# Kernel optimization log

Measured on AMD Instinct MI355X. Metric: run time of the kernel, lower is better.

The kernel has to match this reference:

```python
import jax, jax.numpy as jnp
import numpy as np

MAX_TIMESTEPS = 6
K_WTA = 1
THR_RATE = 0.05
OUT_CHANNELS = 128
TARGET_RATE = K_WTA / OUT_CHANNELS


def setup_inputs() -> dict:
    key = jax.random.key(0)
    kx, kw = jax.random.split(key)
    x = jax.random.normal(kx, (8, 128, 64, 64), dtype=jnp.float32)
    W = jax.random.normal(kw, (128, 256, 11, 11), dtype=jnp.float32)
    # per-output-filter L2 normalization as in __init__
    W = W / (1e-10 + jnp.sqrt(jnp.sum(W * W, axis=(1, 2, 3), keepdims=True)))
    return {"x": x, "W": W}


def _conv_same(x_in, W):
    return jax.lax.conv_general_dilated(
        x_in, W, window_strides=(1, 1), padding="SAME",
        dimension_numbers=("NCHW", "OIHW", "NCHW"))


def reference(x, W):
    B, C, H, Wd = x.shape
    Cout = W.shape[0]

    z0 = jnp.zeros((B, Cout, H, Wd), dtype=x.dtype)  # zeros_like(x), channels match
    b0 = jnp.zeros((1, Cout, 1, 1), dtype=x.dtype)

    def step(carry, t):
        z_prev, b = carry
        x_in = jnp.concatenate([x, z_prev], axis=1)          # [B, 2C, H, W]
        prelimy = _conv_same(x_in, W)                         # [B, Cout, H, W]
        realy = prelimy - b
        # EMA blend with previous (binarized) activation for t > 0
        realy = jnp.where(t > 0, 0.5 * realy + 0.5 * z_prev, realy)
        # k-WTA with k=1 over channel dim: keep only per-pixel channel max, binarize
        thr = jnp.max(realy, axis=1, keepdims=True)
        masked = jnp.where(realy < thr, 0.0, realy)
        z = (masked > 0).astype(x.dtype)
        # running sparsity-controlled bias update
        rate = jnp.mean(z, axis=(0, 2, 3)).reshape(1, -1, 1, 1)
        b = b + THR_RATE * (rate - TARGET_RATE)
        x_in_new = jnp.concatenate([x, z], axis=1)
        change = jnp.mean(jnp.abs(x_in - x_in_new))           # F.l1_loss
        return (z, b), (change, z)

    (_, _), (changes, zs) = jax.lax.scan(step, (z0, b0), jnp.arange(MAX_TIMESTEPS))
    features = jnp.transpose(zs, (1, 0, 2, 3, 4))             # [B, T, Cout, H, W]
    return changes, features
```

## Files before the change

### kernel.cpp

```cpp
#include <hip/hip_runtime.h>

typedef double d4 __attribute__((ext_vector_type(4)));

static constexpr int BN = 8;
static constexpr int CX = 128;
static constexpr int CO = 128;
static constexpr int HH = 64;
static constexpr int WW = 64;
static constexpr int KT = 121;
static constexpr int NPIX = HH * WW;
static constexpr int TOTPIX = BN * NPIX;

__global__ __launch_bounds__(128) void k_wt(const float* __restrict__ W,
                                            float* __restrict__ WxT,
                                            float* __restrict__ WzT) {
  int blk  = blockIdx.x;
  int part = blk >> 7;
  int ci   = blk & 127;
  int co   = threadIdx.x;
  const float* src = &W[((co * 256) + part * 128 + ci) * KT];
  float* dst = (part ? WzT : WxT) + ci * KT * 128 + co;
#pragma unroll 11
  for (int k = 0; k < KT; ++k) dst[k * 128] = src[k];
}

__global__ __launch_bounds__(256, 4) void k_conv(const float* __restrict__ x,
                                                 const float* __restrict__ WxT,
                                                 double* __restrict__ base) {
  int blk = blockIdx.x;
  int cog = blk & 7;
  int wt  = (blk >> 3) & 3;
  int ht  = (blk >> 5) & 3;
  int b   = blk >> 7;
  int H0 = ht * 16, W0 = wt * 16, CO0 = cog * 16;

  int tid  = threadIdx.x;
  int lane = tid & 63;
  int wv   = tid >> 6;
  int lg   = lane >> 4;
  int lc   = lane & 15;

  __shared__ double xs[42 * 28];
  __shared__ double wsl[124 * 16];
  __shared__ unsigned offtbl[124];

  if (tid < 124) {
    unsigned off;
    if (tid < 121) {
      int ki = tid / 11, kj = tid - ki * 11;
      off = (unsigned)(ki * 28 + kj);
    } else {
      off = (unsigned)(26 * 28);
    }
    offtbl[tid] = off;
  }
  for (int e = tid; e < 42 * 28; e += 256) xs[e] = 0.0;
  if (tid < 48) wsl[121 * 16 + tid] = 0.0;

  d4 zz = {0., 0., 0., 0.};
  double amu  = (double)lc;
  double bsel = (lg == 0) ? 1.0 : 0.0;
  d4 pr = __builtin_amdgcn_mfma_f64_16x16x4f64(amu, bsel, zz, 0, 0, 0);
  d4 pc = __builtin_amdgcn_mfma_f64_16x16x4f64(bsel, amu, zz, 0, 0, 0);

  int e0 = tid, e1 = tid + 256, e2 = tid + 512;
  bool v0 = false, v1 = false, v2 = false;
  int g0 = 0, g1 = 0, g2 = 0;
  {
    int e = e0; int r = e / 28, cc = e - r * 28;
    int gh = H0 - 5 + r, gw = W0 - 5 + cc;
    v0 = (cc < 26) && ((unsigned)gh < 64u) && ((unsigned)gw < 64u);
    g0 = ((b * CX) * HH + gh) * WW + gw;
  }
  {
    int e = e1; int r = e / 28, cc = e - r * 28;
    int gh = H0 - 5 + r, gw = W0 - 5 + cc;
    v1 = (cc < 26) && ((unsigned)gh < 64u) && ((unsigned)gw < 64u);
    g1 = ((b * CX) * HH + gh) * WW + gw;
  }
  if (e2 < 728) {
    int e = e2; int r = e / 28, cc = e - r * 28;
    int gh = H0 - 5 + r, gw = W0 - 5 + cc;
    v2 = (cc < 26) && ((unsigned)gh < 64u) && ((unsigned)gw < 64u);
    g2 = ((b * CX) * HH + gh) * WW + gw;
  }
  bool wact = (tid < 242);
  int wk = tid >> 1;
  int wgoff = wk * 128 + CO0 + (tid & 1) * 8;

  float xv0 = 0.f, xv1 = 0.f, xv2 = 0.f;
  float4 wva = {0, 0, 0, 0}, wvb = {0, 0, 0, 0};

  {
    if (v0) xv0 = x[g0];
    if (v1) xv1 = x[g1];
    if (v2) xv2 = x[g2];
    if (wact) {
      wva = *reinterpret_cast<const float4*>(&WxT[wgoff]);
      wvb = *reinterpret_cast<const float4*>(&WxT[wgoff + 4]);
    }
    if (e0 < 728) xs[e0] = v0 ? (double)xv0 : 0.0;
    if (e1 < 728) xs[e1] = v1 ? (double)xv1 : 0.0;
    if (e2 < 728) xs[e2] = v2 ? (double)xv2 : 0.0;
    if (wact) {
      double* dst = &wsl[wk * 16 + (tid & 1) * 8];
      dst[0] = (double)wva.x; dst[1] = (double)wva.y;
      dst[2] = (double)wva.z; dst[3] = (double)wva.w;
      dst[4] = (double)wvb.x; dst[5] = (double)wvb.y;
      dst[6] = (double)wvb.z; dst[7] = (double)wvb.w;
    }
  }
  __syncthreads();

  d4 acc0 = {0., 0., 0., 0.};
  d4 acc1 = {0., 0., 0., 0.};
  d4 acc2 = {0., 0., 0., 0.};
  d4 acc3 = {0., 0., 0., 0.};

  unsigned xbase = (unsigned)(wv * 112 + lc);

  for (int ci = 0; ci < CX; ++ci) {
    if (ci < CX - 1) {
      int xo = (ci + 1) * (HH * WW);
      int wo = (ci + 1) * (KT * 128);
      if (v0) xv0 = x[g0 + xo];
      if (v1) xv1 = x[g1 + xo];
      if (v2) xv2 = x[g2 + xo];
      if (wact) {
        wva = *reinterpret_cast<const float4*>(&WxT[wo + wgoff]);
        wvb = *reinterpret_cast<const float4*>(&WxT[wo + wgoff + 4]);
      }
    }

#pragma unroll 31
    for (int c = 0; c < 31; ++c) {
      double a = wsl[(unsigned)(c * 64 + lg * 16 + lc)];
      unsigned off = offtbl[(unsigned)(c * 4 + lg)];
      const double* bp = &xs[xbase + off];
      double b0 = bp[0];
      double b1 = bp[28];
      double b2 = bp[56];
      double b3 = bp[84];
      acc0 = __builtin_amdgcn_mfma_f64_16x16x4f64(a, b0, acc0, 0, 0, 0);
      acc1 = __builtin_amdgcn_mfma_f64_16x16x4f64(a, b1, acc1, 0, 0, 0);
      acc2 = __builtin_amdgcn_mfma_f64_16x16x4f64(a, b2, acc2, 0, 0, 0);
      acc3 = __builtin_amdgcn_mfma_f64_16x16x4f64(a, b3, acc3, 0, 0, 0);
    }
    __syncthreads();

    if (ci < CX - 1) {
      if (e0 < 728) xs[e0] = v0 ? (double)xv0 : 0.0;
      if (e1 < 728) xs[e1] = v1 ? (double)xv1 : 0.0;
      if (e2 < 728) xs[e2] = v2 ? (double)xv2 : 0.0;
      if (wact) {
        double* dst = &wsl[wk * 16 + (tid & 1) * 8];
        dst[0] = (double)wva.x; dst[1] = (double)wva.y;
        dst[2] = (double)wva.z; dst[3] = (double)wva.w;
        dst[4] = (double)wvb.x; dst[5] = (double)wvb.y;
        dst[6] = (double)wvb.z; dst[7] = (double)wvb.w;
      }
      __syncthreads();
    }
  }

  int hbase = H0 + wv * 4;
#pragma unroll
  for (int i = 0; i < 4; ++i) {
    int co = CO0 + (int)pr[i];
    int wc = W0 + (int)pc[i];
    double* dst = &base[((size_t)b * NPIX + hbase * 64 + wc) * 128 + co];
    dst[0 * 8192] = acc0[i];
    dst[1 * 8192] = acc1[i];
    dst[2 * 8192] = acc2[i];
    dst[3 * 8192] = acc3[i];
  }
}

__global__ __launch_bounds__(256) void k_step(
    const double* __restrict__ base, const float* __restrict__ WzT,
    const unsigned int* __restrict__ counts,
    unsigned int* __restrict__ countsT,
    unsigned int* __restrict__ chgT,
    const unsigned char* __restrict__ widxPrev,
    unsigned char* __restrict__ widxCur,
    const float* __restrict__ zf, int t) {
  int wv   = threadIdx.x >> 6;
  int lane = threadIdx.x & 63;
  int pix  = (blockIdx.x << 2) + wv;
  int b  = pix >> 12;
  int hw = pix & 4095;
  int h = hw >> 6, w = hw & 63;
  int co0 = lane << 1;

  __shared__ int nbrS[4][121];

  double bias0 = 0.0, bias1 = 0.0;
  for (int s = 0; s < t; ++s) {
    double r0 = (double)counts[s * 128 + co0]     * (1.0 / 32768.0);
    double r1 = (double)counts[s * 128 + co0 + 1] * (1.0 / 32768.0);
    bias0 += 0.05 * (r0 - 1.0 / 128.0);
    bias1 += 0.05 * (r1 - 1.0 / 128.0);
  }

  if (t > 0) {
#pragma unroll
    for (int q = 0; q < 2; ++q) {
      int k = lane + q * 64;
      if (k < 121) {
        int ki = k / 11, kj = k - ki * 11;
        int nh = h + ki - 5, nw = w + kj - 5;
        int c = 255;
        if ((unsigned)nh < 64u && (unsigned)nw < 64u)
          c = (int)widxPrev[(b << 12) + (nh << 6) + nw];
        nbrS[wv][k] = c;
      }
    }
  }
  __syncthreads();

  double realy0, realy1;
  {
    double2 bb =
        *reinterpret_cast<const double2*>(&base[(size_t)pix * 128 + co0]);
    realy0 = bb.x;
    realy1 = bb.y;
  }

  const float2* zf2 = reinterpret_cast<const float2*>(zf);

  int wpc = 255;
  if (t > 0) {
    const int* nb = nbrS[wv];
    wpc = nb[60];
    double a0 = 0, a1 = 0, a2 = 0, a3 = 0;
    double b0 = 0, b1 = 0, b2 = 0, b3 = 0;
#pragma unroll 6
    for (int k = 0; k < 120; k += 4) {
      int c0 = nb[k], c1 = nb[k + 1], c2 = nb[k + 2], c3 = nb[k + 3];
      const float2* p0 = (c0 < 128)
          ? reinterpret_cast<const float2*>(&WzT[((c0 * KT + k) << 7) + co0])
          : zf2;
      const float2* p1 = (c1 < 128)
          ? reinterpret_cast<const float2*>(&WzT[((c1 * KT + k + 1) << 7) + co0])
          : zf2;
      const float2* p2 = (c2 < 128)
          ? reinterpret_cast<const float2*>(&WzT[((c2 * KT + k + 2) << 7) + co0])
          : zf2;
      const float2* p3 = (c3 < 128)
          ? reinterpret_cast<const float2*>(&WzT[((c3 * KT + k + 3) << 7) + co0])
          : zf2;
      float2 f0 = *p0, f1 = *p1, f2 = *p2, f3 = *p3;
      a0 += (double)f0.x; b0 += (double)f0.y;
      a1 += (double)f1.x; b1 += (double)f1.y;
      a2 += (double)f2.x; b2 += (double)f2.y;
      a3 += (double)f3.x; b3 += (double)f3.y;
    }
    int cl = nb[120];
    const float2* pl = (cl < 128)
        ? reinterpret_cast<const float2*>(&WzT[((cl * KT + 120) << 7) + co0])
        : zf2;
    float2 fl = *pl;
    a0 += (double)fl.x; b0 += (double)fl.y;
    realy0 += (a0 + a1) + (a2 + a3);
    realy1 += (b0 + b1) + (b2 + b3);
  }

  realy0 -= bias0;
  realy1 -= bias1;
  if (t > 0) {
    realy0 = 0.5 * realy0 + ((wpc == co0)     ? 0.5 : 0.0);
    realy1 = 0.5 * realy1 + ((wpc == co0 + 1) ? 0.5 : 0.0);
  }

  double m = fmax(realy0, realy1);
#pragma unroll
  for (int s = 1; s < 64; s <<= 1) m = fmax(m, __shfl_xor(m, s, 64));

  bool z0 = (realy0 == m) && (realy0 > 0.0);
  bool z1 = (realy1 == m) && (realy1 > 0.0);
  int cand = z0 ? co0 : (z1 ? (co0 + 1) : 255);
#pragma unroll
  for (int s = 1; s < 64; s <<= 1) {
    int o = __shfl_xor(cand, s, 64);
    cand = (o < cand) ? o : cand;
  }

  if (lane == 0) {
    int wi = cand;
    widxCur[pix] = (unsigned char)wi;
    if (wi < 128) atomicAdd(&countsT[wi], 1u);
    if (wpc != wi)
      atomicAdd(chgT, (unsigned)((wpc != 255) + (wi != 255)));
  }
}

__global__ __launch_bounds__(64) void k_ch(const unsigned int* __restrict__ chg,
                                           float* __restrict__ outCh) {
  int t = threadIdx.x;
  if (t < 6) outCh[t] = (float)((double)chg[t] * (1.0 / 8388608.0));
}

__global__ __launch_bounds__(256) void k_feat(const unsigned char* __restrict__ widxA,
                                              float* __restrict__ featBase) {
  int idx = blockIdx.x * 256 + threadIdx.x;
  int hw4 = idx & 1023;
  int co  = (idx >> 10) & 127;
  int bt  = idx >> 17;
  int t = bt % 6, b = bt / 6;
  const unsigned char* wp = &widxA[(size_t)(t * BN + b) * 4096 + hw4 * 4];
  float4 o;
  o.x = (wp[0] == co) ? 1.f : 0.f;
  o.y = (wp[1] == co) ? 1.f : 0.f;
  o.z = (wp[2] == co) ? 1.f : 0.f;
  o.w = (wp[3] == co) ? 1.f : 0.f;
  *reinterpret_cast<float4*>(&featBase[(size_t)idx * 4]) = o;
}

extern "C" void kernel_launch(void* const* d_in, const int* in_sizes, int n_in,
                              void* d_out, int out_size, void* d_ws, size_t ws_size,
                              hipStream_t stream) {
  const float* x = (const float*)d_in[0];
  const float* W = (const float*)d_in[1];
  float* out = (float*)d_out;

  char* ws = (char*)d_ws;
  float* WxT = (float*)ws;
  float* WzT = (float*)(ws + 7929856);
  double* base = (double*)(ws + 2 * 7929856);
  char* p = ws + 2 * 7929856 + 33554432;
  unsigned int* counts = (unsigned int*)p; p += 6 * 128 * 4;
  unsigned int* chg = (unsigned int*)p;    p += 128;
  float* zf = (float*)p;                   p += 64;
  unsigned char* widxA = (unsigned char*)p;

  hipMemsetAsync(counts, 0, 3264, stream);

  k_wt<<<256, 128, 0, stream>>>(W, WxT, WzT);
  k_conv<<<1024, 256, 0, stream>>>(x, WxT, base);

  for (int t = 0; t < 6; ++t) {
    unsigned char* wc = widxA + (size_t)t * TOTPIX;
    const unsigned char* wp = (t > 0) ? (widxA + (size_t)(t - 1) * TOTPIX)
                                      : widxA;
    k_step<<<8192, 256, 0, stream>>>(base, WzT, counts, counts + t * 128,
                                     chg + t, wp, wc, zf, t);
  }
  k_ch<<<1, 64, 0, stream>>>(chg, out);
  k_feat<<<24576, 256, 0, stream>>>(widxA, out + 6);
}
```

Measured before the change: 3.001 ms.

## Double-buffer conv input tile, load weights to registers, pack two pixels per wave

```diff
diff --git a/kernel.cpp b/kernel.cpp
--- a/kernel.cpp
+++ b/kernel.cpp
@@ -40,8 +40,7 @@
   int lg   = lane >> 4;
   int lc   = lane & 15;
 
-  __shared__ double xs[42 * 28];
-  __shared__ double wsl[124 * 16];
+  __shared__ double xs[2][42 * 28];
   __shared__ unsigned offtbl[124];
 
   if (tid < 124) {
@@ -54,8 +53,7 @@
     }
     offtbl[tid] = off;
   }
-  for (int e = tid; e < 42 * 28; e += 256) xs[e] = 0.0;
-  if (tid < 48) wsl[121 * 16 + tid] = 0.0;
+  for (int e = tid; e < 2 * 42 * 28; e += 256) (&xs[0][0])[e] = 0.0;
 
   d4 zz = {0., 0., 0., 0.};
   double amu  = (double)lc;
@@ -84,31 +82,16 @@
     v2 = (cc < 26) && ((unsigned)gh < 64u) && ((unsigned)gw < 64u);
     g2 = ((b * CX) * HH + gh) * WW + gw;
   }
-  bool wact = (tid < 242);
-  int wk = tid >> 1;
-  int wgoff = wk * 128 + CO0 + (tid & 1) * 8;
 
   float xv0 = 0.f, xv1 = 0.f, xv2 = 0.f;
-  float4 wva = {0, 0, 0, 0}, wvb = {0, 0, 0, 0};
 
   {
     if (v0) xv0 = x[g0];
     if (v1) xv1 = x[g1];
     if (v2) xv2 = x[g2];
-    if (wact) {
-      wva = *reinterpret_cast<const float4*>(&WxT[wgoff]);
-      wvb = *reinterpret_cast<const float4*>(&WxT[wgoff + 4]);
-    }
-    if (e0 < 728) xs[e0] = v0 ? (double)xv0 : 0.0;
-    if (e1 < 728) xs[e1] = v1 ? (double)xv1 : 0.0;
-    if (e2 < 728) xs[e2] = v2 ? (double)xv2 : 0.0;
-    if (wact) {
-      double* dst = &wsl[wk * 16 + (tid & 1) * 8];
-      dst[0] = (double)wva.x; dst[1] = (double)wva.y;
-      dst[2] = (double)wva.z; dst[3] = (double)wva.w;
-      dst[4] = (double)wvb.x; dst[5] = (double)wvb.y;
-      dst[6] = (double)wvb.z; dst[7] = (double)wvb.w;
-    }
+    if (e0 < 728) xs[0][e0] = v0 ? (double)xv0 : 0.0;
+    if (e1 < 728) xs[0][e1] = v1 ? (double)xv1 : 0.0;
+    if (e2 < 728) xs[0][e2] = v2 ? (double)xv2 : 0.0;
   }
   __syncthreads();
 
@@ -118,50 +101,55 @@
   d4 acc3 = {0., 0., 0., 0.};
 
   unsigned xbase = (unsigned)(wv * 112 + lc);
-
-  for (int ci = 0; ci < CX; ++ci) {
-    if (ci < CX - 1) {
-      int xo = (ci + 1) * (HH * WW);
-      int wo = (ci + 1) * (KT * 128);
-      if (v0) xv0 = x[g0 + xo];
-      if (v1) xv1 = x[g1 + xo];
-      if (v2) xv2 = x[g2 + xo];
-      if (wact) {
-        wva = *reinterpret_cast<const float4*>(&WxT[wo + wgoff]);
-        wvb = *reinterpret_cast<const float4*>(&WxT[wo + wgoff + 4]);
-      }
-    }
-
-#pragma unroll 31
-    for (int c = 0; c < 31; ++c) {
-      double a = wsl[(unsigned)(c * 64 + lg * 16 + lc)];
-      unsigned off = offtbl[(unsigned)(c * 4 + lg)];
-      const double* bp = &xs[xbase + off];
-      double b0 = bp[0];
-      double b1 = bp[28];
-      double b2 = bp[56];
-      double b3 = bp[84];
-      acc0 = __builtin_amdgcn_mfma_f64_16x16x4f64(a, b0, acc0, 0, 0, 0);
-      acc1 = __builtin_amdgcn_mfma_f64_16x16x4f64(a, b1, acc1, 0, 0, 0);
-      acc2 = __builtin_amdgcn_mfma_f64_16x16x4f64(a, b2, acc2, 0, 0, 0);
-      acc3 = __builtin_amdgcn_mfma_f64_16x16x4f64(a, b3, acc3, 0, 0, 0);
-    }
-    __syncthreads();
-
-    if (ci < CX - 1) {
-      if (e0 < 728) xs[e0] = v0 ? (double)xv0 : 0.0;
-      if (e1 < 728) xs[e1] = v1 ? (double)xv1 : 0.0;
-      if (e2 < 728) xs[e2] = v2 ? (double)xv2 : 0.0;
-      if (wact) {
-        double* dst = &wsl[wk * 16 + (tid & 1) * 8];
-        dst[0] = (double)wva.x; dst[1] = (double)wva.y;
-        dst[2] = (double)wva.z; dst[3] = (double)wva.w;
-        dst[4] = (double)wvb.x; dst[5] = (double)wvb.y;
-        dst[6] = (double)wvb.z; dst[7] = (double)wvb.w;
-      }
-      __syncthreads();
-    }
-  }
+  double* xA = &xs[0][0];
+  double* xB = &xs[1][0];
+
+#define CONV_STEP(CI, XRD, XWR, LAST)                                        \
+  {                                                                          \
+    const float* wci = WxT + (CI) * (KT * 128) + CO0 + lc + lg * 128;        \
+    const float* wcl = WxT + (CI) * (KT * 128) + 120 * 128 + CO0 + lc;       \
+    float wf[31];                                                            \
+    _Pragma("unroll")                                                        \
+    for (int c = 0; c < 30; ++c) wf[c] = wci[c * 512];                       \
+    {                                                                        \
+      float vl = wcl[0];                                                     \
+      wf[30] = (lg == 0) ? vl : 0.0f;        \
+    }                                                                        \
+    if (!(LAST)) {                                                           \
+      int xo = ((CI) + 1) * (HH * WW);                                       \
+      if (v0) xv0 = x[g0 + xo];                                              \
+      if (v1) xv1 = x[g1 + xo];                                              \
+      if (v2) xv2 = x[g2 + xo];                                              \
+    }                                                                        \
+    _Pragma("unroll")                                                        \
+    for (int c = 0; c < 31; ++c) {                                           \
+      double a = (double)wf[c];                                              \
+      unsigned off = offtbl[c * 4 + lg];                                     \
+      const double* bp = &(XRD)[xbase + off];                                \
+      double b0 = bp[0];                                                     \
+      double b1 = bp[28];                                                    \
+      double b2 = bp[56];                                                    \
+      double b3 = bp[84];                                                    \
+      acc0 = __builtin_amdgcn_mfma_f64_16x16x4f64(a, b0, acc0, 0, 0, 0);     \
+      acc1 = __builtin_amdgcn_mfma_f64_16x16x4f64(a, b1, acc1, 0, 0, 0);     \
+      acc2 = __builtin_amdgcn_mfma_f64_16x16x4f64(a, b2, acc2, 0, 0, 0);     \
+      acc3 = __builtin_amdgcn_mfma_f64_16x16x4f64(a, b3, acc3, 0, 0, 0);     \
+    }                                                                        \
+    if (!(LAST)) {                                                           \
+      if (e0 < 728) (XWR)[e0] = v0 ? (double)xv0 : 0.0;                      \
+      if (e1 < 728) (XWR)[e1] = v1 ? (double)xv1 : 0.0;                      \
+      if (e2 < 728) (XWR)[e2] = v2 ? (double)xv2 : 0.0;                      \
+    }                                                                        \
+    __syncthreads();                                                         \
+  }
+
+  for (int ci = 0; ci < 126; ci += 2) {
+    CONV_STEP(ci, xA, xB, false)
+    CONV_STEP(ci + 1, xB, xA, false)
+  }
+  CONV_STEP(126, xA, xB, false)
+  CONV_STEP(127, xB, xA, true)
+#undef CONV_STEP
 
   int hbase = H0 + wv * 4;
 #pragma unroll
@@ -186,106 +174,118 @@
     const float* __restrict__ zf, int t) {
   int wv   = threadIdx.x >> 6;
   int lane = threadIdx.x & 63;
-  int pix  = (blockIdx.x << 2) + wv;
+  int hp   = lane >> 5;
+  int l32  = lane & 31;
+  int slot = (wv << 1) + hp;
+  int pix  = (blockIdx.x << 3) + slot;
   int b  = pix >> 12;
   int hw = pix & 4095;
   int h = hw >> 6, w = hw & 63;
-  int co0 = lane << 1;
-
-  __shared__ int nbrS[4][121];
-
-  double bias0 = 0.0, bias1 = 0.0;
+  int co0 = l32 << 2;
+
+  __shared__ int nbrS[8][121];
+
+  double bias0 = 0.0, bias1 = 0.0, bias2 = 0.0, bias3 = 0.0;
   for (int s = 0; s < t; ++s) {
-    double r0 = (double)counts[s * 128 + co0]     * (1.0 / 32768.0);
-    double r1 = (double)counts[s * 128 + co0 + 1] * (1.0 / 32768.0);
-    bias0 += 0.05 * (r0 - 1.0 / 128.0);
-    bias1 += 0.05 * (r1 - 1.0 / 128.0);
+    uint4 cv = *reinterpret_cast<const uint4*>(&counts[s * 128 + co0]);
+    bias0 += 0.05 * ((double)cv.x * (1.0 / 32768.0) - 1.0 / 128.0);
+    bias1 += 0.05 * ((double)cv.y * (1.0 / 32768.0) - 1.0 / 128.0);
+    bias2 += 0.05 * ((double)cv.z * (1.0 / 32768.0) - 1.0 / 128.0);
+    bias3 += 0.05 * ((double)cv.w * (1.0 / 32768.0) - 1.0 / 128.0);
   }
 
   if (t > 0) {
 #pragma unroll
-    for (int q = 0; q < 2; ++q) {
-      int k = lane + q * 64;
+    for (int q = 0; q < 4; ++q) {
+      int k = l32 + q * 32;
       if (k < 121) {
         int ki = k / 11, kj = k - ki * 11;
         int nh = h + ki - 5, nw = w + kj - 5;
         int c = 255;
         if ((unsigned)nh < 64u && (unsigned)nw < 64u)
           c = (int)widxPrev[(b << 12) + (nh << 6) + nw];
-        nbrS[wv][k] = c;
+        nbrS[slot][k] = c;
       }
     }
   }
   __syncthreads();
 
-  double realy0, realy1;
+  double r0, r1, r2, r3;
   {
-    double2 bb =
-        *reinterpret_cast<const double2*>(&base[(size_t)pix * 128 + co0]);
-    realy0 = bb.x;
-    realy1 = bb.y;
-  }
-
-  const float2* zf2 = reinterpret_cast<const float2*>(zf);
-
+    const double* bp_ = &base[(size_t)pix * 128 + co0];
+    double2 bb0 = *reinterpret_cast<const double2*>(bp_);
+    double2 bb1 = *reinterpret_cast<const double2*>(bp_ + 2);
+    r0 = bb0.x; r1 = bb0.y; r2 = bb1.x; r3 = bb1.y;
+  }
+
+  const float4* zf4 = reinterpret_cast<const float4*>(zf);
   int wpc = 255;
   if (t > 0) {
-    const int* nb = nbrS[wv];
+    const int* nb = nbrS[slot];
     wpc = nb[60];
-    double a0 = 0, a1 = 0, a2 = 0, a3 = 0;
-    double b0 = 0, b1 = 0, b2 = 0, b3 = 0;
+    double ap[4][4] = {};
 #pragma unroll 6
     for (int k = 0; k < 120; k += 4) {
       int c0 = nb[k], c1 = nb[k + 1], c2 = nb[k + 2], c3 = nb[k + 3];
-      const float2* p0 = (c0 < 128)
-          ? reinterpret_cast<const float2*>(&WzT[((c0 * KT + k) << 7) + co0])
-          : zf2;
-      const float2* p1 = (c1 < 128)
-          ? reinterpret_cast<const float2*>(&WzT[((c1 * KT + k + 1) << 7) + co0])
-          : zf2;
-      const float2* p2 = (c2 < 128)
-          ? reinterpret_cast<const float2*>(&WzT[((c2 * KT + k + 2) << 7) + co0])
-          : zf2;
-      const float2* p3 = (c3 < 128)
-          ? reinterpret_cast<const float2*>(&WzT[((c3 * KT + k + 3) << 7) + co0])
-          : zf2;
-      float2 f0 = *p0, f1 = *p1, f2 = *p2, f3 = *p3;
-      a0 += (double)f0.x; b0 += (double)f0.y;
-      a1 += (double)f1.x; b1 += (double)f1.y;
-      a2 += (double)f2.x; b2 += (double)f2.y;
-      a3 += (double)f3.x; b3 += (double)f3.y;
+      const float4* q0 = (c0 < 128)
+          ? reinterpret_cast<const float4*>(&WzT[((c0 * KT + k) << 7) + co0])
+          : zf4;
+      const float4* q1 = (c1 < 128)
+          ? reinterpret_cast<const float4*>(&WzT[((c1 * KT + k + 1) << 7) + co0])
+          : zf4;
+      const float4* q2 = (c2 < 128)
+          ? reinterpret_cast<const float4*>(&WzT[((c2 * KT + k + 2) << 7) + co0])
+          : zf4;
+      const float4* q3 = (c3 < 128)
+          ? reinterpret_cast<const float4*>(&WzT[((c3 * KT + k + 3) << 7) + co0])
+          : zf4;
+      float4 f0 = *q0, f1 = *q1, f2 = *q2, f3 = *q3;
+      ap[0][0] += (double)f0.x; ap[0][1] += (double)f0.y;
+      ap[0][2] += (double)f0.z; ap[0][3] += (double)f0.w;
+      ap[1][0] += (double)f1.x; ap[1][1] += (double)f1.y;
+      ap[1][2] += (double)f1.z; ap[1][3] += (double)f1.w;
+      ap[2][0] += (double)f2.x; ap[2][1] += (double)f2.y;
+      ap[2][2] += (double)f2.z; ap[2][3] += (double)f2.w;
+      ap[3][0] += (double)f3.x; ap[3][1] += (double)f3.y;
+      ap[3][2] += (double)f3.z; ap[3][3] += (double)f3.w;
     }
     int cl = nb[120];
-    const float2* pl = (cl < 128)
-        ? reinterpret_cast<const float2*>(&WzT[((cl * KT + 120) << 7) + co0])
-        : zf2;
-    float2 fl = *pl;
-    a0 += (double)fl.x; b0 += (double)fl.y;
-    realy0 += (a0 + a1) + (a2 + a3);
-    realy1 += (b0 + b1) + (b2 + b3);
-  }
-
-  realy0 -= bias0;
-  realy1 -= bias1;
+    const float4* ql = (cl < 128)
+        ? reinterpret_cast<const float4*>(&WzT[((cl * KT + 120) << 7) + co0])
+        : zf4;
+    float4 fl = *ql;
+    ap[0][0] += (double)fl.x; ap[0][1] += (double)fl.y;
+    ap[0][2] += (double)fl.z; ap[0][3] += (double)fl.w;
+    r0 += (ap[0][0] + ap[1][0]) + (ap[2][0] + ap[3][0]);
+    r1 += (ap[0][1] + ap[1][1]) + (ap[2][1] + ap[3][1]);
+    r2 += (ap[0][2] + ap[1][2]) + (ap[2][2] + ap[3][2]);
+    r3 += (ap[0][3] + ap[1][3]) + (ap[2][3] + ap[3][3]);
+  }
+
+  r0 -= bias0; r1 -= bias1; r2 -= bias2; r3 -= bias3;
   if (t > 0) {
-    realy0 = 0.5 * realy0 + ((wpc == co0)     ? 0.5 : 0.0);
-    realy1 = 0.5 * realy1 + ((wpc == co0 + 1) ? 0.5 : 0.0);
-  }
-
-  double m = fmax(realy0, realy1);
+    r0 = 0.5 * r0 + ((wpc == co0)     ? 0.5 : 0.0);
+    r1 = 0.5 * r1 + ((wpc == co0 + 1) ? 0.5 : 0.0);
+    r2 = 0.5 * r2 + ((wpc == co0 + 2) ? 0.5 : 0.0);
+    r3 = 0.5 * r3 + ((wpc == co0 + 3) ? 0.5 : 0.0);
+  }
+
+  double m = fmax(fmax(r0, r1), fmax(r2, r3));
 #pragma unroll
-  for (int s = 1; s < 64; s <<= 1) m = fmax(m, __shfl_xor(m, s, 64));
-
-  bool z0 = (realy0 == m) && (realy0 > 0.0);
-  bool z1 = (realy1 == m) && (realy1 > 0.0);
-  int cand = z0 ? co0 : (z1 ? (co0 + 1) : 255);
+  for (int s = 1; s < 32; s <<= 1) m = fmax(m, __shfl_xor(m, s, 32));
+
+  int cand = 255;
+  if ((r3 == m) && (r3 > 0.0)) cand = co0 + 3;
+  if ((r2 == m) && (r2 > 0.0)) cand = co0 + 2;
+  if ((r1 == m) && (r1 > 0.0)) cand = co0 + 1;
+  if ((r0 == m) && (r0 > 0.0)) cand = co0;
 #pragma unroll
-  for (int s = 1; s < 64; s <<= 1) {
-    int o = __shfl_xor(cand, s, 64);
+  for (int s = 1; s < 32; s <<= 1) {
+    int o = __shfl_xor(cand, s, 32);
     cand = (o < cand) ? o : cand;
   }
 
-  if (lane == 0) {
+  if (l32 == 0) {
     int wi = cand;
     widxCur[pix] = (unsigned char)wi;
     if (wi < 128) atomicAdd(&countsT[wi], 1u);
@@ -342,7 +342,7 @@
     unsigned char* wc = widxA + (size_t)t * TOTPIX;
     const unsigned char* wp = (t > 0) ? (widxA + (size_t)(t - 1) * TOTPIX)
                                       : widxA;
-    k_step<<<8192, 256, 0, stream>>>(base, WzT, counts, counts + t * 128,
+    k_step<<<4096, 256, 0, stream>>>(base, WzT, counts, counts + t * 128,
                                      chg + t, wp, wc, zf, t);
   }
   k_ch<<<1, 64, 0, stream>>>(chg, out);
```

Result: faster. 2.786 ms (-7.2%).
